# Kernel optimization log

Measured on AMD Instinct MI355X. Metric: run time of the kernel, lower is better.

Reference implementation:

```python
import jax, jax.numpy as jnp
import numpy as np

V, E, H, T = 50000, 128, 256, 9
H2 = H // 2
B, S = 128, 512


def setup_inputs() -> dict:
    key = jax.random.key(0)
    ks = jax.random.split(key, 12)
    sc = 0.05
    return {
        "x": jax.random.randint(ks[0], (B, S), 0, V, dtype=jnp.int64) if False else jax.random.randint(ks[0], (B, S), 0, V).astype(jnp.int64),
        "mask": jnp.ones((B, S), dtype=jnp.int32),
        "embed": jax.random.normal(ks[1], (V, E), jnp.float32) * sc,
        "W_ih_f": jax.random.normal(ks[2], (4 * H2, E), jnp.float32) * sc,
        "W_hh_f": jax.random.normal(ks[3], (4 * H2, H2), jnp.float32) * sc,
        "b_f": jax.random.normal(ks[4], (4 * H2,), jnp.float32) * sc,
        "W_ih_b": jax.random.normal(ks[5], (4 * H2, E), jnp.float32) * sc,
        "W_hh_b": jax.random.normal(ks[6], (4 * H2, H2), jnp.float32) * sc,
        "b_b": jax.random.normal(ks[7], (4 * H2,), jnp.float32) * sc,
        "W_out": jax.random.normal(ks[8], (T, H), jnp.float32) * sc,
        "b_out": jax.random.normal(ks[9], (T,), jnp.float32) * sc,
        "start_trans": jax.random.normal(ks[10], (T,), jnp.float32) * sc,
        "trans": jax.random.normal(ks[11], (T, T), jnp.float32) * sc,
        "end_trans": jax.random.normal(jax.random.fold_in(key, 99), (T,), jnp.float32) * sc,
    }


def _lstm_dir(xg, W_hh, reverse):
    # xg: [B,S,4*H2] precomputed input projections (+bias)
    if reverse:
        xg = xg[:, ::-1]
    b = xg.shape[0]
    h0 = jnp.zeros((b, H2), xg.dtype)

    def step(carry, xt):
        h, c = carry
        g = xt + h @ W_hh.T
        i, f, gg, o = jnp.split(g, 4, axis=-1)
        c = jax.nn.sigmoid(f) * c + jax.nn.sigmoid(i) * jnp.tanh(gg)
        h = jax.nn.sigmoid(o) * jnp.tanh(c)
        return (h, c), h

    _, hs = jax.lax.scan(step, (h0, h0), jnp.swapaxes(xg, 0, 1))
    hs = jnp.swapaxes(hs, 0, 1)  # [B,S,H2]
    if reverse:
        hs = hs[:, ::-1]
    return hs


def _emissions(x, embed, W_ih_f, W_hh_f, b_f, W_ih_b, W_hh_b, b_b, W_out, b_out):
    emb = embed[x]  # [B,S,E]
    xg_f = jnp.einsum('bse,ge->bsg', emb, W_ih_f) + b_f
    xg_b = jnp.einsum('bse,ge->bsg', emb, W_ih_b) + b_b
    h_f = _lstm_dir(xg_f, W_hh_f, False)
    h_b = _lstm_dir(xg_b, W_hh_b, True)
    feats = jnp.concatenate([h_f, h_b], axis=-1)  # [B,S,H]
    return jnp.einsum('bsh,th->bst', feats, W_out) + b_out  # [B,S,T]


def _viterbi(emissions, mask, start_trans, trans, end_trans):
    # emissions [B,S,T], mask [B,S] (1 = valid prefix)
    m = mask.astype(bool)
    score0 = start_trans + emissions[:, 0]  # [B,T]

    def fwd_step(score, inp):
        em_t, m_t = inp  # [B,T], [B]
        nxt = score[:, :, None] + trans[None] + em_t[:, None, :]  # [B,prev,next]
        best = nxt.max(axis=1)
        idx = nxt.argmax(axis=1).astype(jnp.int32)  # [B,T] backpointers
        score = jnp.where(m_t[:, None], best, score)
        return score, idx

    em_rest = jnp.swapaxes(emissions[:, 1:], 0, 1)  # [S-1,B,T]
    m_rest = jnp.swapaxes(m[:, 1:], 0, 1)  # [S-1,B]
    score, history = jax.lax.scan(fwd_step, score0, (em_rest, m_rest))
    final = score + end_trans
    best_scores = final.max(axis=-1)  # [B]
    cur = final.argmax(axis=-1).astype(jnp.int32)  # [B] tag at last valid step

    def back_step(cur, inp):
        hist_t, m_t = inp  # [B,T], [B]
        tag = jnp.where(m_t, cur, -1)  # -1 pads positions beyond seq end
        prev = jnp.take_along_axis(hist_t, cur[:, None], axis=1)[:, 0]
        cur = jnp.where(m_t, prev, cur)
        return cur, tag

    cur0, tags_rev = jax.lax.scan(back_step, cur, (history[::-1], m_rest[::-1]))
    paths = jnp.concatenate(
        [cur0[:, None], jnp.swapaxes(tags_rev, 0, 1)[:, ::-1]], axis=1)  # [B,S]
    return paths, best_scores


def reference(x, mask, embed, W_ih_f, W_hh_f, b_f, W_ih_b, W_hh_b, b_b,
              W_out, b_out, start_trans, trans, end_trans):
    emissions = _emissions(x, embed, W_ih_f, W_hh_f, b_f,
                           W_ih_b, W_hh_b, b_b, W_out, b_out)
    paths, best_scores = _viterbi(emissions, mask, start_trans, trans, end_trans)
    return paths, best_scores
```

## Files before the change

### kernel.cpp

```cpp
#include <hip/hip_runtime.h>
#include <stdint.h>

#define S_LEN 512
#define NT 9

typedef __attribute__((ext_vector_type(8)))  short          bf16x8;
typedef __attribute__((ext_vector_type(4)))  float          f32x4;
typedef __attribute__((ext_vector_type(16))) unsigned short u16x16;
typedef __attribute__((ext_vector_type(4)))  unsigned int   u32x4;

static __device__ __forceinline__ unsigned short f2bf(float f) {
    union { float f; unsigned u; } c; c.f = f;
    return (unsigned short)((c.u + 0x7fffu + ((c.u >> 16) & 1u)) >> 16);
}
static __device__ __forceinline__ float bf2f(unsigned short h) {
    union { unsigned u; float f; } c; c.u = ((unsigned)h) << 16;
    return c.f;
}
static __device__ __forceinline__ bf16x8 cvt8(const float* p) {
    f32x4 a = *(const f32x4*)p, b = *(const f32x4*)(p + 4);
    bf16x8 fr;
    fr[0]=(short)f2bf(a[0]); fr[1]=(short)f2bf(a[1]); fr[2]=(short)f2bf(a[2]); fr[3]=(short)f2bf(a[3]);
    fr[4]=(short)f2bf(b[0]); fr[5]=(short)f2bf(b[1]); fr[6]=(short)f2bf(b[2]); fr[7]=(short)f2bf(b[3]);
    return fr;
}
static __device__ __forceinline__ float sigf(float x) {
    return __builtin_amdgcn_rcpf(1.0f + __expf(-x));
}
static __device__ __forceinline__ float tanhf_(float x) {
    return 1.0f - 2.0f * __builtin_amdgcn_rcpf(1.0f + __expf(2.0f * x));
}
static __device__ __forceinline__ float sel4(f32x4 a, int l4) {
    float x01 = (l4 & 1) ? a[1] : a[0];
    float x23 = (l4 & 1) ? a[3] : a[2];
    return (l4 & 2) ? x23 : x01;
}

static __device__ __forceinline__ void wg_barrier_lds() {
    asm volatile("s_waitcnt lgkmcnt(0)" ::: "memory");
    __builtin_amdgcn_s_barrier();
    asm volatile("" ::: "memory");
}

__global__ __launch_bounds__(512) void k_xg(
    const int* __restrict__ x, const float* __restrict__ embed,
    const float* __restrict__ Wf, const float* __restrict__ bF,
    const float* __restrict__ Wb, const float* __restrict__ bB,
    unsigned short* __restrict__ xg)
{
    const int dir = blockIdx.y;
    const float* __restrict__ W    = dir ? Wb : Wf;
    const float* __restrict__ bias = dir ? bB : bF;
    const int tid = threadIdx.x;
    const int wv = tid >> 6, L = tid & 63, l15 = L & 15, l4 = L >> 4;
    const int s0 = blockIdx.x * 4;

    bf16x8 Bf[4][4];
    float  bq[4];
#pragma unroll
    for (int q = 0; q < 4; ++q) {
        const int gate = q * 128 + wv * 16 + l15;
        bq[q] = bias[gate];
#pragma unroll
        for (int kt = 0; kt < 4; ++kt)
            Bf[q][kt] = cvt8(W + gate * 128 + kt * 32 + l4 * 8);
    }

    __shared__ int tokL[512];
    __shared__ unsigned short stage[2048];

    tokL[tid] = x[(tid >> 2) * S_LEN + s0 + (tid & 3)];
    const int srow = tid >> 5, scol = tid & 31;
    __syncthreads();

    f32x4 v0 = *(const f32x4*)(embed + (size_t)tokL[srow]      * 128 + scol * 4);
    f32x4 v1 = *(const f32x4*)(embed + (size_t)tokL[16 + srow] * 128 + scol * 4);

    for (int mt = 0; mt < 32; ++mt) {
        const int si = mt >> 3, bt16 = mt & 7;
        wg_barrier_lds();
        {
            unsigned short b4[4];
            b4[0]=f2bf(v0[0]); b4[1]=f2bf(v0[1]); b4[2]=f2bf(v0[2]); b4[3]=f2bf(v0[3]);
            int byte = srow * 256 + ((scol * 8) ^ ((srow & 7) << 4));
            *(uint2*)((char*)stage + byte) = *(const uint2*)b4;
        }
        wg_barrier_lds();
        const int mt2 = (mt < 30) ? (mt + 2) : mt;
        f32x4 v2 = *(const f32x4*)(embed + (size_t)tokL[16 * mt2 + srow] * 128 + scol * 4);

        bf16x8 A[4];
#pragma unroll
        for (int kt = 0; kt < 4; ++kt) {
            int byte = l15 * 256 + ((kt * 64 + l4 * 16) ^ ((l15 & 7) << 4));
            A[kt] = *(const bf16x8*)((const char*)stage + byte);
        }
        unsigned short ov[16];
#pragma unroll
        for (int q = 0; q < 4; ++q) {
            f32x4 acc = { bq[q], bq[q], bq[q], bq[q] };
#pragma unroll
            for (int kt = 0; kt < 4; ++kt)
                acc = __builtin_amdgcn_mfma_f32_16x16x32_bf16(A[kt], Bf[q][kt], acc, 0, 0, 0);
            ov[q*4+0]=f2bf(acc[0]); ov[q*4+1]=f2bf(acc[1]);
            ov[q*4+2]=f2bf(acc[2]); ov[q*4+3]=f2bf(acc[3]);
        }
        const int s = s0 + si;
        unsigned short* dst = xg +
            (((((size_t)s * 2 + dir) * 32 + bt16 * 4 + l4) * 8 + wv) * 256 + l15 * 16);
        *(u32x4*)dst       = *(const u32x4*)&ov[0];
        *(u32x4*)(dst + 8) = *(const u32x4*)&ov[8];
        v0 = v1; v1 = v2;
    }
}

__global__ __launch_bounds__(512) void k_lstm(
    const unsigned short* __restrict__ xg,
    const float* __restrict__ Whf, const float* __restrict__ Whb,
    const float* __restrict__ Wout, float* __restrict__ emp)
{
    const int dir = blockIdx.y, bt = blockIdx.x;
    const float* __restrict__ Wh = dir ? Whb : Whf;
    const int tid = threadIdx.x, w = tid >> 6, L = tid & 63, l15 = L & 15, l4 = L >> 4;

    bf16x8 Bf[4][4];
#pragma unroll
    for (int q = 0; q < 4; ++q)
#pragma unroll
        for (int kt = 0; kt < 4; ++kt)
            Bf[q][kt] = cvt8(Wh + (q * 128 + w * 16 + l15) * 128 + kt * 32 + l4 * 8);

    bf16x8 Of[4];
#pragma unroll
    for (int kt = 0; kt < 4; ++kt) { bf16x8 z;
#pragma unroll
        for (int i = 0; i < 8; ++i) z[i] = 0; Of[kt] = z; }
    if (l15 < NT) {
#pragma unroll
        for (int kt = 0; kt < 4; ++kt)
            Of[kt] = cvt8(Wout + l15 * 256 + dir * 128 + kt * 32 + l4 * 8);
    }

    __shared__ unsigned short hl[2048];
    for (int i = tid; i < 1024; i += 512) ((unsigned*)hl)[i] = 0;

    const int ar = l15 & 3;
    int rdoff[4];
#pragma unroll
    for (int kt = 0; kt < 4; ++kt) {
        int p = (kt * 4 + l4 + 2 * ar) & 15;
        rdoff[kt] = ar * 256 + p * 16;
    }
    const int hc = w * 16 + l15;
    const int wroff = l4 * 256 + (((hc >> 3) + 2 * l4) & 15) * 16 + (hc & 7) * 2;

    float c = 0.f;
    const size_t xstep = (size_t)2 * 32 * 8 * 256;
    const size_t xbase = (((size_t)dir * 32 + bt) * 8 + w) * 256 + l15 * 16;

    u16x16 x0 = *(const u16x16*)(xg + xbase + (size_t)(dir ? 511 : 510 + 1 - 1) * 0 + (size_t)(dir ? 511 : 0) * xstep);
    u16x16 x1 = *(const u16x16*)(xg + xbase + (size_t)(dir ? 510 : 1) * xstep);
    __syncthreads();

    for (int t = 0; t < 512; ++t) {
        const char* bufR = (const char*)hl + (t & 1) * 1024;
        char*       bufW = (char*)hl + ((t & 1) ^ 1) * 1024;

        const int tc = (t < 510) ? (t + 2) : t;
        const int s2 = dir ? (511 - tc) : tc;
        u16x16 x2 = *(const u16x16*)(xg + xbase + (size_t)s2 * xstep);

        bf16x8 A[4];
#pragma unroll
        for (int kt = 0; kt < 4; ++kt)
            A[kt] = *(const bf16x8*)(bufR + rdoff[kt]);

        f32x4 acc[4];
#pragma unroll
        for (int q = 0; q < 4; ++q) {
            f32x4 a0 = { bf2f(x0[q*4+0]), bf2f(x0[q*4+1]), bf2f(x0[q*4+2]), bf2f(x0[q*4+3]) };
#pragma unroll
            for (int kt = 0; kt < 4; ++kt)
                a0 = __builtin_amdgcn_mfma_f32_16x16x32_bf16(A[kt], Bf[q][kt], a0, 0, 0, 0);
            acc[q] = a0;
        }
        if (t > 0 && w == (t & 7)) {
            f32x4 em0 = {0, 0, 0, 0};
#pragma unroll
            for (int kt = 0; kt < 4; ++kt)
                em0 = __builtin_amdgcn_mfma_f32_16x16x32_bf16(A[kt], Of[kt], em0, 0, 0, 0);
            if (l4 == 0 && l15 < NT) {
                const int sp = dir ? (512 - t) : (t - 1);
#pragma unroll
                for (int j = 0; j < 4; ++j)
                    emp[((size_t)(dir * 128 + bt * 4 + j) * 512 + sp) * 9 + l15] = em0[j];
            }
        }
        float ig = sigf(sel4(acc[0], l4));
        float fg = sigf(sel4(acc[1], l4));
        float gg = tanhf_(sel4(acc[2], l4));
        float og = sigf(sel4(acc[3], l4));
        c = fg * c + ig * gg;
        float h = og * tanhf_(c);
        *(unsigned short*)(bufW + wroff) = f2bf(h);
        wg_barrier_lds();
        x0 = x1; x1 = x2;
    }
    if (w == 0) {
        bf16x8 A[4];
#pragma unroll
        for (int kt = 0; kt < 4; ++kt)
            A[kt] = *(const bf16x8*)((const char*)hl + rdoff[kt]);
        f32x4 em0 = {0, 0, 0, 0};
#pragma unroll
        for (int kt = 0; kt < 4; ++kt)
            em0 = __builtin_amdgcn_mfma_f32_16x16x32_bf16(A[kt], Of[kt], em0, 0, 0, 0);
        if (l4 == 0 && l15 < NT) {
            const int sp = dir ? 0 : 511;
#pragma unroll
            for (int j = 0; j < 4; ++j)
                emp[((size_t)(dir * 128 + bt * 4 + j) * 512 + sp) * 9 + l15] = em0[j];
        }
    }
}

__global__ __launch_bounds__(256) void k_viterbi(
    const float* __restrict__ emp, const int* __restrict__ mask,
    const float* __restrict__ bout, const float* __restrict__ startt,
    const float* __restrict__ trans, const float* __restrict__ endt,
    float* __restrict__ out)
{
    const int b = blockIdx.x, tid = threadIdx.x;
    __shared__ float em[512 * 9];
    __shared__ int   msk[512];
    __shared__ unsigned char hist[512 * 9];
    __shared__ unsigned char Gl[32 * 12];
    __shared__ unsigned char bound[32];
    __shared__ int curS;

    const float* pf = emp + (size_t)b * 4608;
    const float* pb = emp + (size_t)(128 + b) * 4608;
    for (int i = tid; i < 4608; i += 256) {
        unsigned q = ((unsigned)i * 7282u) >> 16;
        em[i] = pf[i] + pb[i] + bout[i - 9 * q];
    }
    for (int i = tid; i < 512; i += 256) msk[i] = mask[b * 512 + i];
    __syncthreads();

    if (tid < 64) {
        const int k = (tid < NT) ? tid : 0;
        float trk[9];
#pragma unroll
        for (int j = 0; j < NT; ++j) trk[j] = trans[j * 9 + k];
        float score = startt[k] + em[k];
        for (int t = 1; t < 512; ++t) {
            float v[9];
#pragma unroll
            for (int j = 0; j < NT; ++j) v[j] = __shfl(score, j, 64) + trk[j];
            float m01 = fmaxf(v[0], v[1]), m23 = fmaxf(v[2], v[3]);
            float m45 = fmaxf(v[4], v[5]), m67 = fmaxf(v[6], v[7]);
            float m = fmaxf(fmaxf(fmaxf(m01, m23), fmaxf(m45, m67)), v[8]);
            int bi = 0;
#pragma unroll
            for (int j = 8; j >= 0; --j) if (v[j] == m) bi = j;
            if (msk[t]) score = m + em[t * 9 + k];
            if (tid < NT) hist[t * 9 + tid] = (unsigned char)bi;
        }
        float fin = score + endt[k];
        float bs = -3e38f; int cur = 0;
#pragma unroll
        for (int j = 0; j < NT; ++j) {
            float vv = __shfl(fin, j, 64);
            if (vv > bs) { bs = vv; cur = j; }
        }
        if (tid == 0) { curS = cur; out[65536 + b] = bs; }
    }
    __syncthreads();

    if (tid < 32) {
        const int m = tid;
        int G[9];
#pragma unroll
        for (int k = 0; k < NT; ++k) G[k] = k;
        const int hi = (m == 31) ? 511 : (16 * m + 16);
        for (int t = hi; t >= 16 * m + 1; --t) {
            if (msk[t]) {
#pragma unroll
                for (int k = 0; k < NT; ++k) G[k] = hist[t * 9 + G[k]];
            }
        }
#pragma unroll
        for (int k = 0; k < NT; ++k) Gl[m * 12 + k] = (unsigned char)G[k];
    }
    __syncthreads();

    if (tid == 0) {
        int e = curS;
        bound[31] = (unsigned char)e;
        for (int m = 31; m >= 1; --m) { e = Gl[m * 12 + e]; bound[m - 1] = (unsigned char)e; }
        out[(size_t)b * 512] = (float)Gl[0 * 12 + e];
    }
    __syncthreads();

    if (tid < 32) {
        const int m = tid;
        int ccur = bound[m];
        const int hi = (m == 31) ? 511 : (16 * m + 16);
        for (int t = hi; t >= 16 * m + 1; --t) {
            const int mt = msk[t];
            out[(size_t)b * 512 + t] = (float)(mt ? ccur : -1);
            if (mt) ccur = hist[t * 9 + ccur];
        }
    }
}

extern "C" void kernel_launch(void* const* d_in, const int* in_sizes, int n_in,
                              void* d_out, int out_size, void* d_ws, size_t ws_size,
                              hipStream_t stream) {
    const int*   x      = (const int*)d_in[0];
    const int*   mask   = (const int*)d_in[1];
    const float* embed  = (const float*)d_in[2];
    const float* Wihf   = (const float*)d_in[3];
    const float* Whhf   = (const float*)d_in[4];
    const float* bf_    = (const float*)d_in[5];
    const float* Wihb   = (const float*)d_in[6];
    const float* Whhb   = (const float*)d_in[7];
    const float* bb_    = (const float*)d_in[8];
    const float* Wout   = (const float*)d_in[9];
    const float* bout   = (const float*)d_in[10];
    const float* startt = (const float*)d_in[11];
    const float* trans  = (const float*)d_in[12];
    const float* endt   = (const float*)d_in[13];

    unsigned short* xg  = (unsigned short*)d_ws;
    float*          emp = (float*)((char*)d_ws + (size_t)134217728);
    float*          out = (float*)d_out;

    k_xg     <<<dim3(128, 2), 512, 0, stream>>>(x, embed, Wihf, bf_, Wihb, bb_, xg);
    k_lstm   <<<dim3(32, 2),  512, 0, stream>>>(xg, Whhf, Whhb, Wout, emp);
    k_viterbi<<<128,          256, 0, stream>>>(emp, mask, bout, startt, trans, endt, out);
}
```

Before: 495.2 us.

## Split emission projection out of LSTM recurrence and regrid input projection

After: 462.7 us. -6.6%, faster.

```diff
diff --git a/kernel.cpp b/kernel.cpp
--- a/kernel.cpp
+++ b/kernel.cpp
@@ -48,12 +48,11 @@
     const float* __restrict__ Wb, const float* __restrict__ bB,
     unsigned short* __restrict__ xg)
 {
-    const int dir = blockIdx.y;
+    const int dir = blockIdx.y, s = blockIdx.x;
     const float* __restrict__ W    = dir ? Wb : Wf;
     const float* __restrict__ bias = dir ? bB : bF;
     const int tid = threadIdx.x;
     const int wv = tid >> 6, L = tid & 63, l15 = L & 15, l4 = L >> 4;
-    const int s0 = blockIdx.x * 4;
 
     bf16x8 Bf[4][4];
     float  bq[4];
@@ -66,18 +65,17 @@
             Bf[q][kt] = cvt8(W + gate * 128 + kt * 32 + l4 * 8);
     }
 
-    __shared__ int tokL[512];
+    __shared__ int tokL[128];
     __shared__ unsigned short stage[2048];
 
-    tokL[tid] = x[(tid >> 2) * S_LEN + s0 + (tid & 3)];
+    if (tid < 128) tokL[tid] = x[tid * S_LEN + s];
     const int srow = tid >> 5, scol = tid & 31;
     __syncthreads();
 
     f32x4 v0 = *(const f32x4*)(embed + (size_t)tokL[srow]      * 128 + scol * 4);
     f32x4 v1 = *(const f32x4*)(embed + (size_t)tokL[16 + srow] * 128 + scol * 4);
 
-    for (int mt = 0; mt < 32; ++mt) {
-        const int si = mt >> 3, bt16 = mt & 7;
+    for (int bt16 = 0; bt16 < 8; ++bt16) {
         wg_barrier_lds();
         {
             unsigned short b4[4];
@@ -86,8 +84,8 @@
             *(uint2*)((char*)stage + byte) = *(const uint2*)b4;
         }
         wg_barrier_lds();
-        const int mt2 = (mt < 30) ? (mt + 2) : mt;
-        f32x4 v2 = *(const f32x4*)(embed + (size_t)tokL[16 * mt2 + srow] * 128 + scol * 4);
+        const int nt2 = (bt16 < 6) ? (bt16 + 2) : bt16;
+        f32x4 v2 = *(const f32x4*)(embed + (size_t)tokL[nt2 * 16 + srow] * 128 + scol * 4);
 
         bf16x8 A[4];
 #pragma unroll
@@ -105,7 +103,6 @@
             ov[q*4+0]=f2bf(acc[0]); ov[q*4+1]=f2bf(acc[1]);
             ov[q*4+2]=f2bf(acc[2]); ov[q*4+3]=f2bf(acc[3]);
         }
-        const int s = s0 + si;
         unsigned short* dst = xg +
             (((((size_t)s * 2 + dir) * 32 + bt16 * 4 + l4) * 8 + wv) * 256 + l15 * 16);
         *(u32x4*)dst       = *(const u32x4*)&ov[0];
@@ -117,7 +114,7 @@
 __global__ __launch_bounds__(512) void k_lstm(
     const unsigned short* __restrict__ xg,
     const float* __restrict__ Whf, const float* __restrict__ Whb,
-    const float* __restrict__ Wout, float* __restrict__ emp)
+    unsigned short* __restrict__ feats)
 {
     const int dir = blockIdx.y, bt = blockIdx.x;
     const float* __restrict__ Wh = dir ? Whb : Whf;
@@ -130,17 +127,6 @@
         for (int kt = 0; kt < 4; ++kt)
             Bf[q][kt] = cvt8(Wh + (q * 128 + w * 16 + l15) * 128 + kt * 32 + l4 * 8);
 
-    bf16x8 Of[4];
-#pragma unroll
-    for (int kt = 0; kt < 4; ++kt) { bf16x8 z;
-#pragma unroll
-        for (int i = 0; i < 8; ++i) z[i] = 0; Of[kt] = z; }
-    if (l15 < NT) {
-#pragma unroll
-        for (int kt = 0; kt < 4; ++kt)
-            Of[kt] = cvt8(Wout + l15 * 256 + dir * 128 + kt * 32 + l4 * 8);
-    }
-
     __shared__ unsigned short hl[2048];
     for (int i = tid; i < 1024; i += 512) ((unsigned*)hl)[i] = 0;
 
@@ -157,8 +143,9 @@
     float c = 0.f;
     const size_t xstep = (size_t)2 * 32 * 8 * 256;
     const size_t xbase = (((size_t)dir * 32 + bt) * 8 + w) * 256 + l15 * 16;
-
-    u16x16 x0 = *(const u16x16*)(xg + xbase + (size_t)(dir ? 511 : 510 + 1 - 1) * 0 + (size_t)(dir ? 511 : 0) * xstep);
+    unsigned short* fptr = feats + ((size_t)(bt * 4 + l4) * 512) * 256 + dir * 128 + hc;
+
+    u16x16 x0 = *(const u16x16*)(xg + xbase + (size_t)(dir ? 511 : 0) * xstep);
     u16x16 x1 = *(const u16x16*)(xg + xbase + (size_t)(dir ? 510 : 1) * xstep);
     __syncthreads();
 
@@ -183,18 +170,6 @@
             for (int kt = 0; kt < 4; ++kt)
                 a0 = __builtin_amdgcn_mfma_f32_16x16x32_bf16(A[kt], Bf[q][kt], a0, 0, 0, 0);
             acc[q] = a0;
-        }
-        if (t > 0 && w == (t & 7)) {
-            f32x4 em0 = {0, 0, 0, 0};
-#pragma unroll
-            for (int kt = 0; kt < 4; ++kt)
-                em0 = __builtin_amdgcn_mfma_f32_16x16x32_bf16(A[kt], Of[kt], em0, 0, 0, 0);
-            if (l4 == 0 && l15 < NT) {
-                const int sp = dir ? (512 - t) : (t - 1);
-#pragma unroll
-                for (int j = 0; j < 4; ++j)
-                    emp[((size_t)(dir * 128 + bt * 4 + j) * 512 + sp) * 9 + l15] = em0[j];
-            }
         }
         float ig = sigf(sel4(acc[0], l4));
         float fg = sigf(sel4(acc[1], l4));
@@ -202,24 +177,54 @@
         float og = sigf(sel4(acc[3], l4));
         c = fg * c + ig * gg;
         float h = og * tanhf_(c);
-        *(unsigned short*)(bufW + wroff) = f2bf(h);
+        unsigned short hb = f2bf(h);
+        *(unsigned short*)(bufW + wroff) = hb;
+        const int s_pos = dir ? (511 - t) : t;
+        fptr[(size_t)s_pos * 256] = hb;
         wg_barrier_lds();
         x0 = x1; x1 = x2;
     }
-    if (w == 0) {
+}
+
+__global__ __launch_bounds__(256) void k_emis(
+    const unsigned short* __restrict__ feats,
+    const float* __restrict__ Wout, float* __restrict__ emp)
+{
+    const int tid = threadIdx.x;
+    const int wid = blockIdx.x * 4 + (tid >> 6);
+    const int L = tid & 63, l15 = L & 15, l4 = L >> 4;
+    const int b = wid >> 5, sg = wid & 31;
+
+    bf16x8 Of[2][4];
+#pragma unroll
+    for (int d = 0; d < 2; ++d)
+#pragma unroll
+        for (int kt = 0; kt < 4; ++kt) { bf16x8 z;
+#pragma unroll
+            for (int i = 0; i < 8; ++i) z[i] = 0; Of[d][kt] = z; }
+    if (l15 < NT) {
+#pragma unroll
+        for (int d = 0; d < 2; ++d)
+#pragma unroll
+            for (int kt = 0; kt < 4; ++kt)
+                Of[d][kt] = cvt8(Wout + l15 * 256 + d * 128 + kt * 32 + l4 * 8);
+    }
+
+    const unsigned short* frow = feats + ((size_t)b * 512 + sg * 16 + l15) * 256;
+#pragma unroll
+    for (int d = 0; d < 2; ++d) {
         bf16x8 A[4];
 #pragma unroll
         for (int kt = 0; kt < 4; ++kt)
-            A[kt] = *(const bf16x8*)((const char*)hl + rdoff[kt]);
+            A[kt] = *(const bf16x8*)(frow + d * 128 + kt * 32 + l4 * 8);
         f32x4 em0 = {0, 0, 0, 0};
 #pragma unroll
         for (int kt = 0; kt < 4; ++kt)
-            em0 = __builtin_amdgcn_mfma_f32_16x16x32_bf16(A[kt], Of[kt], em0, 0, 0, 0);
-        if (l4 == 0 && l15 < NT) {
-            const int sp = dir ? 0 : 511;
+            em0 = __builtin_amdgcn_mfma_f32_16x16x32_bf16(A[kt], Of[d][kt], em0, 0, 0, 0);
+        if (l15 < NT) {
 #pragma unroll
             for (int j = 0; j < 4; ++j)
-                emp[((size_t)(dir * 128 + bt * 4 + j) * 512 + sp) * 9 + l15] = em0[j];
+                emp[((size_t)(d * 128 + b) * 512 + sg * 16 + l4 * 4 + j) * 9 + l15] = em0[j];
         }
     }
 }
@@ -332,11 +337,13 @@
     const float* trans  = (const float*)d_in[12];
     const float* endt   = (const float*)d_in[13];
 
-    unsigned short* xg  = (unsigned short*)d_ws;
-    float*          emp = (float*)((char*)d_ws + (size_t)134217728);
-    float*          out = (float*)d_out;
-
-    k_xg     <<<dim3(128, 2), 512, 0, stream>>>(x, embed, Wihf, bf_, Wihb, bb_, xg);
-    k_lstm   <<<dim3(32, 2),  512, 0, stream>>>(xg, Whhf, Whhb, Wout, emp);
+    unsigned short* xg    = (unsigned short*)d_ws;
+    float*          emp   = (float*)((char*)d_ws + (size_t)134217728);
+    unsigned short* feats = (unsigned short*)((char*)d_ws + (size_t)138936320);
+    float*          out   = (float*)d_out;
+
+    k_xg     <<<dim3(512, 2), 512, 0, stream>>>(x, embed, Wihf, bf_, Wihb, bb_, xg);
+    k_lstm   <<<dim3(32, 2),  512, 0, stream>>>(xg, Whhf, Whhb, feats);
+    k_emis   <<<1024,         256, 0, stream>>>(feats, Wout, emp);
     k_viterbi<<<128,          256, 0, stream>>>(emp, mask, bout, startt, trans, endt, out);
 }
```
